# Performance work log

Measured on AMD Instinct MI355X. Metric: run time of the kernel, lower is better.

Reference implementation:

```python
import jax, jax.numpy as jnp
import numpy as np

B, D, H, L, A, NH = 32768, 512, 512, 64, 4, 4
HD = L // NH  # head dim
TEMPS = jnp.array([1.5, 0.5, 1.0, 0.8], dtype=jnp.float32)  # explorer/exploiter/validator/integrator


def setup_inputs() -> dict:
    key = jax.random.key(0)
    ks = jax.random.split(key, 32)
    s = 0.05
    n = lambda k, shp: jax.random.normal(k, shp, dtype=jnp.float32) * s
    return {
        'x': jax.random.normal(ks[0], (B, D), dtype=jnp.float32),
        'eps': jax.random.normal(ks[1], (B, A, L), dtype=jnp.float32),
        'W1': n(ks[2], (H, D)), 'b1': n(ks[3], (H,)),
        'W2': n(ks[4], (H, H)), 'b2': n(ks[5], (H,)),
        'muW': n(ks[6], (A, L, H)), 'mub': n(ks[7], (A, L)),
        'lvW': n(ks[8], (A, L, H)), 'lvb': n(ks[9], (A, L)),
        'Wqkv': n(ks[10], (3 * L, L)), 'bqkv': n(ks[11], (3 * L,)),
        'Wo': n(ks[12], (L, L)), 'bo': n(ks[13], (L,)),
        'Wc': n(ks[14], (L, A * L)), 'bc': n(ks[15], (L,)),
        'Wd1': n(ks[16], (H, L)), 'bd1': n(ks[17], (H,)),
        'Wd2': n(ks[18], (H, H)), 'bd2': n(ks[19], (H,)),
        'Wd3': n(ks[20], (D, H)), 'bd3': n(ks[21], (D,)),
    }


def reference(x, eps, W1, b1, W2, b2, muW, mub, lvW, lvb,
              Wqkv, bqkv, Wo, bo, Wc, bc, Wd1, bd1, Wd2, bd2, Wd3, bd3):
    b = x.shape[0]
    # shared encoder backbone: Linear-ReLU-Linear-ReLU
    h = jax.nn.relu(x @ W1.T + b1)
    h = jax.nn.relu(h @ W2.T + b2)
    # per-agent heads, batched over agent axis a
    mus = jnp.einsum('bh,alh->bal', h, muW) + mub                      # (B,A,L)
    logvars = jnp.einsum('bh,alh->bal', h, lvW) + lvb + jnp.log(TEMPS)[:, None]
    std = jnp.exp(0.5 * logvars)
    z = mus + eps * std * TEMPS[:, None]                               # (B,A,L)
    # multihead self-attention across the A agents (seq_len = A)
    qkv = z @ Wqkv.T + bqkv                                            # (B,A,3L)
    q, k, v = jnp.split(qkv, 3, axis=-1)
    q = q.reshape(b, A, NH, HD)
    k = k.reshape(b, A, NH, HD)
    v = v.reshape(b, A, NH, HD)
    scores = jnp.einsum('bqnh,bknh->bnqk', q, k) / jnp.sqrt(jnp.float32(HD))
    attn = jax.nn.softmax(scores, axis=-1)
    ctx = jnp.einsum('bnqk,bknh->bqnh', attn, v).reshape(b, A, L)
    z_att = ctx @ Wo.T + bo                                            # (B,A,L)
    # consensus over flattened agent latents
    z_consensus = z_att.reshape(b, A * L) @ Wc.T + bc                  # (B,L)

    def decode(zz):
        d = jax.nn.relu(zz @ Wd1.T + bd1)
        d = jax.nn.relu(d @ Wd2.T + bd2)
        return d @ Wd3.T + bd3

    x_recon = decode(z_consensus)                                      # (B,D)
    agent_recons = decode(z)                                           # (B,A,D)
    # stack consensus recon with per-agent recons: (B, A+1, D)
    return jnp.concatenate([x_recon[:, None, :], agent_recons], axis=1)
```

## Files before the change

kernel.cpp:

```cpp
#include <hip/hip_runtime.h>

typedef __bf16 bf16_t;
typedef __bf16 bf16x8 __attribute__((ext_vector_type(8)));
typedef __bf16 bf16x4 __attribute__((ext_vector_type(4)));
typedef float  f32x4  __attribute__((ext_vector_type(4)));
typedef float  f32x16 __attribute__((ext_vector_type(16)));

#define MFMA16(a,b,c) __builtin_amdgcn_mfma_f32_16x16x32_bf16((a),(b),(c),0,0,0)
#define MFMA32(a,b,c) __builtin_amdgcn_mfma_f32_32x32x16_bf16((a),(b),(c),0,0,0)
#define GLOBAL_AS __attribute__((address_space(1)))
#define LDS_AS    __attribute__((address_space(3)))
#define MEMFENCE  asm volatile("" ::: "memory")

__device__ __forceinline__ int act_off(int row, int kByte) {
    int byte = (row << 10) + kByte;
    return byte ^ ((row & 15) << 4);
}

__device__ __forceinline__ bf16x8 lds_read8(const bf16_t* base, int row, int k, int rowB) {
    int byte = row * rowB + (k << 1);
    byte ^= ((row & 7) << 4);
    return *(const bf16x8*)((const char*)base + byte);
}
__device__ __forceinline__ void lds_write8B(bf16_t* base, int row, int col, int rowB, bf16x4 v) {
    int byte = row * rowB + (col << 1);
    byte ^= ((row & 7) << 4);
    *(bf16x4*)((char*)base + byte) = v;
}
__device__ __forceinline__ bf16x4 lds_read8B(const bf16_t* base, int row, int col, int rowB) {
    int byte = row * rowB + (col << 1);
    byte ^= ((row & 7) << 4);
    return *(const bf16x4*)((const char*)base + byte);
}
__device__ __forceinline__ void lds_write1(bf16_t* base, int row, int col, int rowB, float v) {
    int byte = row * rowB + (col << 1);
    byte ^= ((row & 7) << 4);
    *(bf16_t*)((char*)base + byte) = (bf16_t)v;
}
__device__ __forceinline__ void lds_write16B(bf16_t* base, int row, int colbyte, int rowB, bf16x8 v) {
    int byte = row * rowB + colbyte;
    byte ^= ((row & 7) << 4);
    *(bf16x8*)((char*)base + byte) = v;
}
__device__ __forceinline__ bf16x8 lds_read16B(const bf16_t* base, int row, int colbyte, int rowB) {
    int byte = row * rowB + colbyte;
    byte ^= ((row & 7) << 4);
    return *(const bf16x8*)((const char*)base + byte);
}

__device__ __forceinline__ void gload_lds16(const void* g, void* l) {
    __builtin_amdgcn_global_load_lds((const GLOBAL_AS void*)g, (LDS_AS void*)l, 16, 0, 0);
}

__device__ __forceinline__ void stageW32(const bf16_t* __restrict__ Wt, int tile,
                                         char* wbuf, int bufIdx, int wave, int lane) {
    const char* s = (const char*)Wt + (size_t)tile * 32768 + wave * 4096 + lane * 16;
    char* d = wbuf + bufIdx * 32768 + wave * 4096;
#pragma unroll
    for (int c = 0; c < 4; ++c)
        gload_lds16(s + c * 1024, d + c * 1024);
}

template<int NS, bool CONT, int TB>
__device__ __forceinline__ void layer_gl(f32x4 (&acc)[4][4],
    const bf16_t* act, char* wbuf,
    const bf16_t* __restrict__ Wt, const bf16_t* __restrict__ Wn,
    int wave, int lane, int n0, int l15, int lhi)
{
#pragma unroll
    for (int s = 0; s < NS; ++s) {
        if (s == NS - 1 && !CONT) {
            asm volatile("s_waitcnt vmcnt(0)" ::: "memory");
        } else {
            asm volatile("s_waitcnt vmcnt(4)" ::: "memory");
        }
        __builtin_amdgcn_s_barrier();
        if (s + 2 < NS)  stageW32(Wt, s + 2,      wbuf, (TB + s + 2) % 3, wave, lane);
        else if (CONT)   stageW32(Wn, s + 2 - NS, wbuf, (TB + s + 2) % 3, wave, lane);
        const char* bb = wbuf + ((TB + s) % 3) * 32768 + lhi * 8192;
        bf16x8 a[4], b[4];
#pragma unroll
        for (int cf = 0; cf < 4; ++cf)
            b[cf] = *(const bf16x8*)(bb + (n0 + cf * 16 + l15) * 16);
#pragma unroll
        for (int rf = 0; rf < 4; ++rf)
            a[rf] = lds_read8(act, rf * 16 + l15, s * 32 + lhi * 8, 1024);
#pragma unroll
        for (int rf = 0; rf < 4; ++rf)
#pragma unroll
            for (int cf = 0; cf < 4; ++cf)
                acc[rf][cf] = MFMA16(b[cf], a[rf], acc[rf][cf]);
    }
}

__device__ __forceinline__ void zero4(f32x4 (&acc)[4][4]) {
#pragma unroll
    for (int rf = 0; rf < 4; ++rf)
#pragma unroll
        for (int cf = 0; cf < 4; ++cf)
            acc[rf][cf] = f32x4{0.f, 0.f, 0.f, 0.f};
}

template<bool RELU>
__device__ __forceinline__ void epi_lds16(const f32x4 (&acc)[4][4], const float* __restrict__ bias,
    bf16_t* dst, int n0, int l15, int lhi)
{
#pragma unroll
    for (int cf = 0; cf < 4; ++cf) {
        const int c0 = n0 + cf * 16 + lhi * 4;
        float4 b4 = *(const float4*)(bias + c0);
#pragma unroll
        for (int rf = 0; rf < 4; ++rf) {
            float v0 = acc[rf][cf][0] + b4.x;
            float v1 = acc[rf][cf][1] + b4.y;
            float v2 = acc[rf][cf][2] + b4.z;
            float v3 = acc[rf][cf][3] + b4.w;
            if (RELU) {
                v0 = fmaxf(v0, 0.f); v1 = fmaxf(v1, 0.f);
                v2 = fmaxf(v2, 0.f); v3 = fmaxf(v3, 0.f);
            }
            bf16x4 p = { (bf16_t)v0, (bf16_t)v1, (bf16_t)v2, (bf16_t)v3 };
            lds_write8B(dst, rf * 16 + l15, c0, 1024, p);
        }
    }
}

__device__ __forceinline__ void compute_step(f32x16 (&acc)[2][4],
    const bf16_t* act, const char* wbuf, int s, int wm, int wn, int l31, int kg)
{
    bf16x8 a[2], b[4];
#pragma unroll
    for (int cc = 0; cc < 4; ++cc)
        b[cc] = *(const bf16x8*)(wbuf + kg * 8192 + (wn * 128 + cc * 32 + l31) * 16);
#pragma unroll
    for (int rr = 0; rr < 2; ++rr)
        a[rr] = *(const bf16x8*)((const char*)act +
                    act_off(wm * 64 + rr * 32 + l31, s * 32 + kg * 16));
#pragma unroll
    for (int rr = 0; rr < 2; ++rr)
#pragma unroll
        for (int cc = 0; cc < 4; ++cc)
            acc[rr][cc] = MFMA32(b[cc], a[rr], acc[rr][cc]);
}

template<int NS>
__device__ __forceinline__ void layer_rs(f32x16 (&acc)[2][4],
    const bf16_t* act, char* wbuf, const bf16_t* __restrict__ Wt,
    int t, int wave, int lane, int wm, int wn, int l31, int kg)
{
    const char* gb = (const char*)Wt;
    {
        const char* s0 = gb + wave * 2048 + lane * 16;
        char* d0 = wbuf + wave * 2048;
        gload_lds16(s0, d0);
        gload_lds16(s0 + 1024, d0 + 1024);
    }
    MEMFENCE;
    uint4 rA0, rA1, rB0, rB1;
    rA0 = *(const uint4*)(gb + 16384 + t * 16);
    rA1 = *(const uint4*)(gb + 16384 + 8192 + t * 16);
    asm volatile("s_waitcnt vmcnt(0)" ::: "memory");
    __builtin_amdgcn_s_barrier();

#pragma unroll
    for (int p = 0; p < NS / 2; ++p) {
        {
            const int s = 2 * p;
            compute_step(acc, act, wbuf + (s & 1) * 16384, s, wm, wn, l31, kg);
            if (s + 2 < NS) {
                MEMFENCE;
                rB0 = *(const uint4*)(gb + (size_t)(s + 2) * 16384 + t * 16);
                rB1 = *(const uint4*)(gb + (size_t)(s + 2) * 16384 + 8192 + t * 16);
                MEMFENCE;
            }
            if (s + 1 < NS) {
                if (s + 2 < NS) asm volatile("s_waitcnt vmcnt(2)" ::: "memory");
                else            asm volatile("s_waitcnt vmcnt(0)" ::: "memory");
                char* nb = wbuf + ((s + 1) & 1) * 16384;
                *(uint4*)(nb + t * 16) = rA0;
                *(uint4*)(nb + 8192 + t * 16) = rA1;
                asm volatile("s_waitcnt lgkmcnt(0)" ::: "memory");
            }
            __builtin_amdgcn_s_barrier();
        }
        {
            const int s = 2 * p + 1;
            compute_step(acc, act, wbuf + (s & 1) * 16384, s, wm, wn, l31, kg);
            if (s + 2 < NS) {
                MEMFENCE;
                rA0 = *(const uint4*)(gb + (size_t)(s + 2) * 16384 + t * 16);
                rA1 = *(const uint4*)(gb + (size_t)(s + 2) * 16384 + 8192 + t * 16);
                MEMFENCE;
            }
            if (s + 1 < NS) {
                if (s + 2 < NS) asm volatile("s_waitcnt vmcnt(2)" ::: "memory");
                else            asm volatile("s_waitcnt vmcnt(0)" ::: "memory");
                char* nb = wbuf + ((s + 1) & 1) * 16384;
                *(uint4*)(nb + t * 16) = rB0;
                *(uint4*)(nb + 8192 + t * 16) = rB1;
                asm volatile("s_waitcnt lgkmcnt(0)" ::: "memory");
            }
            __builtin_amdgcn_s_barrier();
        }
    }
}

__device__ __forceinline__ void zero32(f32x16 (&acc)[2][4]) {
#pragma unroll
    for (int rr = 0; rr < 2; ++rr)
#pragma unroll
        for (int cc = 0; cc < 4; ++cc)
#pragma unroll
            for (int i = 0; i < 16; ++i) acc[rr][cc][i] = 0.f;
}

template<bool RELU>
__device__ __forceinline__ void epi_lds32(const f32x16 (&acc)[2][4], const float* __restrict__ bias,
    bf16_t* act, int wm, int wn, int l31, int kg)
{
#pragma unroll
    for (int cc = 0; cc < 4; ++cc)
#pragma unroll
    for (int q = 0; q < 4; ++q) {
        const int c0 = wn * 128 + cc * 32 + q * 8 + kg * 4;
        float4 b4 = *(const float4*)(bias + c0);
#pragma unroll
        for (int rr = 0; rr < 2; ++rr) {
            float v0 = acc[rr][cc][q * 4 + 0] + b4.x;
            float v1 = acc[rr][cc][q * 4 + 1] + b4.y;
            float v2 = acc[rr][cc][q * 4 + 2] + b4.z;
            float v3 = acc[rr][cc][q * 4 + 3] + b4.w;
            if (RELU) {
                v0 = fmaxf(v0, 0.f); v1 = fmaxf(v1, 0.f);
                v2 = fmaxf(v2, 0.f); v3 = fmaxf(v3, 0.f);
            }
            bf16x4 p = { (bf16_t)v0, (bf16_t)v1, (bf16_t)v2, (bf16_t)v3 };
            *(bf16x4*)((char*)act + act_off(wm * 64 + rr * 32 + l31, c0 * 2)) = p;
        }
    }
}
__device__ __forceinline__ void epi_global32(const f32x16 (&acc)[2][4], const float* __restrict__ bias,
    float* __restrict__ out, long r0, int wm, int wn, int l31, int kg)
{
#pragma unroll
    for (int cc = 0; cc < 4; ++cc)
#pragma unroll
    for (int q = 0; q < 4; ++q) {
        const int c0 = wn * 128 + cc * 32 + q * 8 + kg * 4;
        float4 b4 = *(const float4*)(bias + c0);
#pragma unroll
        for (int rr = 0; rr < 2; ++rr) {
            float4 o = { acc[rr][cc][q * 4 + 0] + b4.x, acc[rr][cc][q * 4 + 1] + b4.y,
                         acc[rr][cc][q * 4 + 2] + b4.z, acc[rr][cc][q * 4 + 3] + b4.w };
            *(float4*)(out + (r0 + wm * 64 + rr * 32 + l31) * 512 + c0) = o;
        }
    }
}

__device__ __forceinline__ void decode32(int m, int& n, int& k) {
    int s = m >> 14, r = m & 16383;
    int kg = r >> 12, q = r & 4095;
    n = q >> 3;
    k = (s << 5) + (kg << 3) + (q & 7);
}
__device__ __forceinline__ void decode16(int m, int& n, int& k) {
    int s = m >> 13, r = m & 8191;
    int kg = r >> 12, q = r & 4095;
    n = q >> 3;
    k = (s << 4) + (kg << 3) + (q & 7);
}
__global__ __launch_bounds__(256) void cast_kernel(
    const float* __restrict__ W1, const float* __restrict__ W2,
    const float* __restrict__ muW, const float* __restrict__ lvW,
    const float* __restrict__ Wqkv, const float* __restrict__ Wo,
    const float* __restrict__ Wc, const float* __restrict__ Wd1,
    const float* __restrict__ Wd2, const float* __restrict__ Wd3,
    bf16_t* __restrict__ dst)
{
    int i = blockIdx.x * 256 + threadIdx.x;
    float val;
    int n, k;
    if (i < 262144) {
        decode32(i, n, k);                    val = W1[n * 512 + k];
    } else if (i < 524288) {
        decode32(i - 262144, n, k);           val = W2[n * 512 + k];
    } else if (i < 786432) {
        decode32(i - 524288, n, k);
        val = (n < 256) ? muW[n * 512 + k] : lvW[(n - 256) * 512 + k];
    } else if (i < 798720) { val = Wqkv[i - 786432]; }
    else if (i < 802816)   { val = Wo[i - 798720]; }
    else if (i < 819200)   { val = Wc[i - 802816]; }
    else if (i < 851968) {
        decode16(i - 819200, n, k);           val = Wd1[n * 64 + k];
    } else if (i < 1114112) {
        decode16(i - 851968, n, k);           val = Wd2[n * 512 + k];
    } else {
        decode16(i - 1114112, n, k);          val = Wd3[n * 512 + k];
    }
    dst[i] = (bf16_t)val;
}

__global__ __launch_bounds__(512, 2) void enc_kernel(
    const float* __restrict__ x, const float* __restrict__ eps,
    const bf16_t* __restrict__ W1t, const float* __restrict__ b1,
    const bf16_t* __restrict__ W2t, const float* __restrict__ b2,
    const bf16_t* __restrict__ Ht,  const float* __restrict__ mub,
    const float* __restrict__ lvb,  bf16_t* __restrict__ zout)
{
    __shared__ bf16_t act[64 * 512];
    __shared__ alignas(16) char wbuf[3 * 32768];
    const int t = threadIdx.x;
    const int wave = t >> 6, lane = t & 63, l15 = lane & 15, lhi = lane >> 4;
    const int n0 = wave * 64;
    const size_t r0 = (size_t)blockIdx.x * 64;

    stageW32(W1t, 0, wbuf, 0, wave, lane);
    stageW32(W1t, 1, wbuf, 1, wave, lane);

    for (int it = 0; it < 16; ++it) {
        int flat = it * 512 + t;
        int row = flat >> 7, c4 = flat & 127;
        float4 v = ((const float4*)(x + (r0 + row) * 512))[c4];
        bf16x4 h = { (bf16_t)v.x, (bf16_t)v.y, (bf16_t)v.z, (bf16_t)v.w };
        int byte = (row << 10) + (c4 << 3);
        byte ^= ((row & 7) << 4);
        *(bf16x4*)((char*)act + byte) = h;
    }
    asm volatile("s_waitcnt lgkmcnt(0)" ::: "memory");

    f32x4 acc[4][4];
    zero4(acc);
    layer_gl<16, true, 0>(acc, act, wbuf, W1t, W2t, wave, lane, n0, l15, lhi);
    __builtin_amdgcn_s_barrier();
    epi_lds16<true>(acc, b1, act, n0, l15, lhi);
    asm volatile("s_waitcnt lgkmcnt(0)" ::: "memory");
    __builtin_amdgcn_s_barrier();

    zero4(acc);
    layer_gl<16, true, 1>(acc, act, wbuf, W2t, Ht, wave, lane, n0, l15, lhi);
    __builtin_amdgcn_s_barrier();
    epi_lds16<true>(acc, b2, act, n0, l15, lhi);
    asm volatile("s_waitcnt lgkmcnt(0)" ::: "memory");
    __builtin_amdgcn_s_barrier();

    zero4(acc);
    layer_gl<16, false, 2>(acc, act, wbuf, Ht, (const bf16_t*)nullptr, wave, lane, n0, l15, lhi);
    __builtin_amdgcn_s_barrier();
    epi_lds16<false>(acc, (n0 < 256) ? (mub + 0) : (lvb - 256), act, n0, l15, lhi);
    asm volatile("s_waitcnt lgkmcnt(0)" ::: "memory");
    __builtin_amdgcn_s_barrier();

    const int cc = (t & 63) * 4;
    const int ag = cc >> 6;
    const float tp = (ag == 0) ? 1.8371173070873836f
                   : (ag == 1) ? 0.35355339059327373f
                   : (ag == 2) ? 1.0f
                               : 0.7155417527999327f;
    const int rb = t >> 6;
    for (int it = 0; it < 8; ++it) {
        int row = it * 8 + rb;
        bf16x4 mu4 = lds_read8B(act, row, cc, 1024);
        bf16x4 lv4 = lds_read8B(act, row, cc + 256, 1024);
        float4 ep4 = *(const float4*)(eps + (r0 + row) * 256 + cc);
        bf16x4 zo;
        zo[0] = (bf16_t)fmaf(ep4.x * tp, expf(0.5f * (float)lv4[0]), (float)mu4[0]);
        zo[1] = (bf16_t)fmaf(ep4.y * tp, expf(0.5f * (float)lv4[1]), (float)mu4[1]);
        zo[2] = (bf16_t)fmaf(ep4.z * tp, expf(0.5f * (float)lv4[2]), (float)mu4[2]);
        zo[3] = (bf16_t)fmaf(ep4.w * tp, expf(0.5f * (float)lv4[3]), (float)mu4[3]);
        *(bf16x4*)(zout + (r0 + row) * 256 + cc) = zo;
    }
}

__global__ __launch_bounds__(512) void attn_kernel(
    const bf16_t* __restrict__ z,
    const bf16_t* __restrict__ Wqkvb, const float* __restrict__ bqkv,
    const bf16_t* __restrict__ Wob,   const float* __restrict__ bo,
    const bf16_t* __restrict__ Wcb,   const float* __restrict__ bc,
    bf16_t* __restrict__ zcb)
{
    __shared__ bf16_t zt[256 * 64];
    __shared__ bf16_t qt[256 * 192];
    const int t = threadIdx.x;
    const size_t s0 = (size_t)blockIdx.x * 64;

    for (int it = 0; it < 4; ++it) {
        int ch = it * 512 + t;
        int r = ch >> 3, cc = ch & 7;
        bf16x8 v = *(const bf16x8*)(z + s0 * 256 + r * 64 + cc * 8);
        lds_write16B(zt, r, cc * 16, 128, v);
    }
    __syncthreads();
    const int wave = t >> 6, lane = t & 63, l15 = lane & 15, lhi = lane >> 4;
    const int rbase = wave * 32;

    for (int cc = 0; cc < 4; ++cc) {
        f32x4 acc[2][3] = {};
#pragma unroll
        for (int ks = 0; ks < 2; ++ks) {
            int k = ks * 32 + lhi * 8;
            bf16x8 a0 = lds_read8(zt, rbase + l15, k, 128);
            bf16x8 a1 = lds_read8(zt, rbase + 16 + l15, k, 128);
#pragma unroll
            for (int cf = 0; cf < 3; ++cf) {
                bf16x8 b = *(const bf16x8*)(Wqkvb + (cc * 48 + cf * 16 + l15) * 64 + k);
                acc[0][cf] = MFMA16(a0, b, acc[0][cf]);
                acc[1][cf] = MFMA16(a1, b, acc[1][cf]);
            }
        }
#pragma unroll
        for (int cf = 0; cf < 3; ++cf) {
            int col = cc * 48 + cf * 16 + l15;
            float bs = bqkv[col];
#pragma unroll
            for (int rf = 0; rf < 2; ++rf)
#pragma unroll
                for (int r = 0; r < 4; ++r)
                    lds_write1(qt, rbase + rf * 16 + lhi * 4 + r, col, 384, acc[rf][cf][r] + bs);
        }
    }
    __syncthreads();

    if (t < 256) {
        const int sl = t >> 2, head = t & 3;
        bf16x8 qv[4][2], kv[4][2], vv[4][2];
#pragma unroll
        for (int a2 = 0; a2 < 4; ++a2) {
            int r = sl * 4 + a2;
#pragma unroll
            for (int i = 0; i < 2; ++i) {
                qv[a2][i] = lds_read16B(qt, r, head * 32 + 16 * i, 384);
                kv[a2][i] = lds_read16B(qt, r, 128 + head * 32 + 16 * i, 384);
                vv[a2][i] = lds_read16B(qt, r, 256 + head * 32 + 16 * i, 384);
            }
        }
        float sc[4][4];
#pragma unroll
        for (int qa = 0; qa < 4; ++qa)
#pragma unroll
            for (int ka = 0; ka < 4; ++ka) {
                float s = 0.f;
#pragma unroll
                for (int i = 0; i < 2; ++i)
#pragma unroll
                    for (int j = 0; j < 8; ++j)
                        s += (float)qv[qa][i][j] * (float)kv[ka][i][j];
                sc[qa][ka] = s * 0.25f;
            }
#pragma unroll
        for (int qa = 0; qa < 4; ++qa) {
            float m = fmaxf(fmaxf(sc[qa][0], sc[qa][1]), fmaxf(sc[qa][2], sc[qa][3]));
            float e[4], sum = 0.f;
#pragma unroll
            for (int ka = 0; ka < 4; ++ka) { e[ka] = expf(sc[qa][ka] - m); sum += e[ka]; }
            float inv = 1.f / sum;
#pragma unroll
            for (int i = 0; i < 2; ++i) {
                bf16x8 cv;
#pragma unroll
                for (int j = 0; j < 8; ++j) {
                    float cval = 0.f;
#pragma unroll
                    for (int ka = 0; ka < 4; ++ka) cval += e[ka] * inv * (float)vv[ka][i][j];
                    cv[j] = (bf16_t)cval;
                }
                lds_write16B(zt, sl * 4 + qa, head * 32 + 16 * i, 128, cv);
            }
        }
    }
    __syncthreads();

    {
        f32x4 acc[2][4] = {};
#pragma unroll
        for (int ks = 0; ks < 2; ++ks) {
            int k = ks * 32 + lhi * 8;
            bf16x8 a0 = lds_read8(zt, rbase + l15, k, 128);
            bf16x8 a1 = lds_read8(zt, rbase + 16 + l15, k, 128);
#pragma unroll
            for (int cf = 0; cf < 4; ++cf) {
                bf16x8 b = *(const bf16x8*)(Wob + (cf * 16 + l15) * 64 + k);
                acc[0][cf] = MFMA16(a0, b, acc[0][cf]);
                acc[1][cf] = MFMA16(a1, b, acc[1][cf]);
            }
        }
        __syncthreads();
#pragma unroll
        for (int cf = 0; cf < 4; ++cf) {
            int col = cf * 16 + l15;
            float bs = bo[col];
#pragma unroll
            for (int rf = 0; rf < 2; ++rf)
#pragma unroll
                for (int r = 0; r < 4; ++r)
                    lds_write1(qt, rbase + rf * 16 + lhi * 4 + r, col, 128, acc[rf][cf][r] + bs);
        }
    }
    __syncthreads();

    {
        f32x4 acc2[2] = {};
        const int rfw = wave >> 1, cbase = (wave & 1) * 2;
        const int srow = rfw * 16 + l15;
#pragma unroll
        for (int ks = 0; ks < 8; ++ks) {
            int k = ks * 32 + lhi * 8;
            int byte = (srow << 9) + (k << 1);
            byte ^= ((((srow << 2) + (k >> 6)) & 7) << 4);
            bf16x8 a = *(const bf16x8*)((const char*)qt + byte);
#pragma unroll
            for (int i = 0; i < 2; ++i) {
                bf16x8 b = *(const bf16x8*)(Wcb + ((cbase + i) * 16 + l15) * 256 + k);
                acc2[i] = MFMA16(a, b, acc2[i]);
            }
        }
#pragma unroll
        for (int i = 0; i < 2; ++i) {
            int col = (cbase + i) * 16 + l15;
            float bs = bc[col];
#pragma unroll
            for (int r = 0; r < 4; ++r) {
                int s = (int)(s0) + rfw * 16 + lhi * 4 + r;
                zcb[(size_t)s * 64 + col] = (bf16_t)(acc2[i][r] + bs);
            }
        }
    }
}

__global__ __launch_bounds__(512, 2) void dec_kernel(
    const bf16_t* __restrict__ z, const bf16_t* __restrict__ zc,
    const bf16_t* __restrict__ Wd1t, const float* __restrict__ bd1,
    const bf16_t* __restrict__ Wd2t, const float* __restrict__ bd2,
    const bf16_t* __restrict__ Wd3t, const float* __restrict__ bd3,
    float* __restrict__ out)
{
    __shared__ bf16_t act[128 * 512];
    __shared__ alignas(16) char wbuf[2 * 16384];
    const int t = threadIdx.x;
    const int wave = t >> 6, lane = t & 63, l31 = lane & 31, kg = lane >> 5;
    const int wm = wave >> 2, wn = wave & 3;
    const long r0 = (long)blockIdx.x * 128;

    for (int it = 0; it < 2; ++it) {
        int flat = it * 512 + t;
        int row = flat >> 3, ch = flat & 7;
        long rg = r0 + row;
        int s5 = (int)(rg / 5), j = (int)(rg - (long)s5 * 5);
        const bf16_t* src = (j == 0) ? (zc + (size_t)s5 * 64)
                                     : (z + (size_t)s5 * 256 + (j - 1) * 64);
        bf16x8 v = *(const bf16x8*)(src + ch * 8);
        *(bf16x8*)((char*)act + act_off(row, ch * 16)) = v;
    }
    asm volatile("s_waitcnt lgkmcnt(0)" ::: "memory");

    f32x16 acc[2][4];
    zero32(acc);
    layer_rs<4>(acc, act, wbuf, Wd1t, t, wave, lane, wm, wn, l31, kg);
    epi_lds32<true>(acc, bd1, act, wm, wn, l31, kg);
    asm volatile("s_waitcnt lgkmcnt(0)" ::: "memory");
    __builtin_amdgcn_s_barrier();

    zero32(acc);
    layer_rs<32>(acc, act, wbuf, Wd2t, t, wave, lane, wm, wn, l31, kg);
    epi_lds32<true>(acc, bd2, act, wm, wn, l31, kg);
    asm volatile("s_waitcnt lgkmcnt(0)" ::: "memory");
    __builtin_amdgcn_s_barrier();

    zero32(acc);
    layer_rs<32>(acc, act, wbuf, Wd3t, t, wave, lane, wm, wn, l31, kg);
    epi_global32(acc, bd3, out, r0, wm, wn, l31, kg);
}

extern "C" void kernel_launch(void* const* d_in, const int* in_sizes, int n_in,
                              void* d_out, int out_size, void* d_ws, size_t ws_size,
                              hipStream_t stream) {
    const float* x    = (const float*)d_in[0];
    const float* eps  = (const float*)d_in[1];
    const float* W1   = (const float*)d_in[2];
    const float* b1   = (const float*)d_in[3];
    const float* W2   = (const float*)d_in[4];
    const float* b2   = (const float*)d_in[5];
    const float* muW  = (const float*)d_in[6];
    const float* mub  = (const float*)d_in[7];
    const float* lvW  = (const float*)d_in[8];
    const float* lvb  = (const float*)d_in[9];
    const float* Wqkv = (const float*)d_in[10];
    const float* bqkv = (const float*)d_in[11];
    const float* Wo   = (const float*)d_in[12];
    const float* bo   = (const float*)d_in[13];
    const float* Wc   = (const float*)d_in[14];
    const float* bc   = (const float*)d_in[15];
    const float* Wd1  = (const float*)d_in[16];
    const float* bd1  = (const float*)d_in[17];
    const float* Wd2  = (const float*)d_in[18];
    const float* bd2  = (const float*)d_in[19];
    const float* Wd3  = (const float*)d_in[20];
    const float* bd3  = (const float*)d_in[21];
    float* out = (float*)d_out;

    bf16_t* wsb  = (bf16_t*)d_ws;
    bf16_t* W1t  = wsb + 0;
    bf16_t* W2t  = wsb + 262144;
    bf16_t* Ht   = wsb + 524288;
    bf16_t* Wqkvb= wsb + 786432;
    bf16_t* Wob  = wsb + 798720;
    bf16_t* Wcb  = wsb + 802816;
    bf16_t* Wd1t = wsb + 819200;
    bf16_t* Wd2t = wsb + 851968;
    bf16_t* Wd3t = wsb + 1114112;
    bf16_t* zbuf = wsb + 1376256;
    bf16_t* zcb  = wsb + 9764864;

    cast_kernel<<<dim3(5376), dim3(256), 0, stream>>>(
        W1, W2, muW, lvW, Wqkv, Wo, Wc, Wd1, Wd2, Wd3, wsb);
    enc_kernel<<<dim3(512), dim3(512), 0, stream>>>(
        x, eps, W1t, b1, W2t, b2, Ht, mub, lvb, zbuf);
    attn_kernel<<<dim3(512), dim3(512), 0, stream>>>(
        zbuf, Wqkvb, bqkv, Wob, bo, Wcb, bc, zcb);
    dec_kernel<<<dim3(1280), dim3(512), 0, stream>>>(
        zbuf, zcb, Wd1t, bd1, Wd2t, bd2, Wd3t, bd3, out);
}
```

Baseline: 380.8 us.

## Stream decoder weights directly into registers instead of staging through LDS

The decoder kernel no longer stages each weight K-slice through a double-buffered LDS buffer with per-step barriers. Each wave now loads its own B fragments from global memory straight into registers, two slices ahead, in a layout the cast kernel pre-permutes to match. This removes the LDS weight traffic, the per-step block barriers and 32KB of LDS. In exchange each wave issues its own global loads (duplicated across the two wm waves) and holds more registers, which may hurt latency hiding or occupancy.

```diff
diff --git a/kernel.cpp b/kernel.cpp
--- a/kernel.cpp
+++ b/kernel.cpp
@@ -10,7 +10,6 @@
 #define MFMA32(a,b,c) __builtin_amdgcn_mfma_f32_32x32x16_bf16((a),(b),(c),0,0,0)
 #define GLOBAL_AS __attribute__((address_space(1)))
 #define LDS_AS    __attribute__((address_space(3)))
-#define MEMFENCE  asm volatile("" ::: "memory")
 
 __device__ __forceinline__ int act_off(int row, int kByte) {
     int byte = (row << 10) + kByte;
@@ -125,13 +124,10 @@
     }
 }
 
-__device__ __forceinline__ void compute_step(f32x16 (&acc)[2][4],
-    const bf16_t* act, const char* wbuf, int s, int wm, int wn, int l31, int kg)
-{
-    bf16x8 a[2], b[4];
-#pragma unroll
-    for (int cc = 0; cc < 4; ++cc)
-        b[cc] = *(const bf16x8*)(wbuf + kg * 8192 + (wn * 128 + cc * 32 + l31) * 16);
+__device__ __forceinline__ void dec_mfma(f32x16 (&acc)[2][4],
+    const bf16_t* act, const bf16x8 (&b)[4], int s, int wm, int l31, int kg)
+{
+    bf16x8 a[2];
 #pragma unroll
     for (int rr = 0; rr < 2; ++rr)
         a[rr] = *(const bf16x8*)((const char*)act +
@@ -144,63 +140,41 @@
 }
 
 template<int NS>
-__device__ __forceinline__ void layer_rs(f32x16 (&acc)[2][4],
-    const bf16_t* act, char* wbuf, const bf16_t* __restrict__ Wt,
-    int t, int wave, int lane, int wm, int wn, int l31, int kg)
-{
-    const char* gb = (const char*)Wt;
-    {
-        const char* s0 = gb + wave * 2048 + lane * 16;
-        char* d0 = wbuf + wave * 2048;
-        gload_lds16(s0, d0);
-        gload_lds16(s0 + 1024, d0 + 1024);
-    }
-    MEMFENCE;
-    uint4 rA0, rA1, rB0, rB1;
-    rA0 = *(const uint4*)(gb + 16384 + t * 16);
-    rA1 = *(const uint4*)(gb + 16384 + 8192 + t * 16);
-    asm volatile("s_waitcnt vmcnt(0)" ::: "memory");
-    __builtin_amdgcn_s_barrier();
-
+__device__ __forceinline__ void layer_reg(f32x16 (&acc)[2][4],
+    const bf16_t* act, const bf16_t* __restrict__ Wt,
+    int lane, int wm, int wn, int l31, int kg)
+{
+    const char* gb = (const char*)Wt + wn * 4096 + lane * 16;
+    bf16x8 pA[4], pB[4];
+#pragma unroll
+    for (int c = 0; c < 4; ++c) pA[c] = *(const bf16x8*)(gb + c * 1024);
+#pragma unroll
+    for (int c = 0; c < 4; ++c) pB[c] = *(const bf16x8*)(gb + 16384 + c * 1024);
 #pragma unroll
     for (int p = 0; p < NS / 2; ++p) {
         {
             const int s = 2 * p;
-            compute_step(acc, act, wbuf + (s & 1) * 16384, s, wm, wn, l31, kg);
+            bf16x8 b[4];
+#pragma unroll
+            for (int c = 0; c < 4; ++c) b[c] = pA[c];
             if (s + 2 < NS) {
-                MEMFENCE;
-                rB0 = *(const uint4*)(gb + (size_t)(s + 2) * 16384 + t * 16);
-                rB1 = *(const uint4*)(gb + (size_t)(s + 2) * 16384 + 8192 + t * 16);
-                MEMFENCE;
-            }
-            if (s + 1 < NS) {
-                if (s + 2 < NS) asm volatile("s_waitcnt vmcnt(2)" ::: "memory");
-                else            asm volatile("s_waitcnt vmcnt(0)" ::: "memory");
-                char* nb = wbuf + ((s + 1) & 1) * 16384;
-                *(uint4*)(nb + t * 16) = rA0;
-                *(uint4*)(nb + 8192 + t * 16) = rA1;
-                asm volatile("s_waitcnt lgkmcnt(0)" ::: "memory");
-            }
-            __builtin_amdgcn_s_barrier();
+#pragma unroll
+                for (int c = 0; c < 4; ++c)
+                    pA[c] = *(const bf16x8*)(gb + (size_t)(s + 2) * 16384 + c * 1024);
+            }
+            dec_mfma(acc, act, b, s, wm, l31, kg);
         }
         {
             const int s = 2 * p + 1;
-            compute_step(acc, act, wbuf + (s & 1) * 16384, s, wm, wn, l31, kg);
+            bf16x8 b[4];
+#pragma unroll
+            for (int c = 0; c < 4; ++c) b[c] = pB[c];
             if (s + 2 < NS) {
-                MEMFENCE;
-                rA0 = *(const uint4*)(gb + (size_t)(s + 2) * 16384 + t * 16);
-                rA1 = *(const uint4*)(gb + (size_t)(s + 2) * 16384 + 8192 + t * 16);
-                MEMFENCE;
-            }
-            if (s + 1 < NS) {
-                if (s + 2 < NS) asm volatile("s_waitcnt vmcnt(2)" ::: "memory");
-                else            asm volatile("s_waitcnt vmcnt(0)" ::: "memory");
-                char* nb = wbuf + ((s + 1) & 1) * 16384;
-                *(uint4*)(nb + t * 16) = rB0;
-                *(uint4*)(nb + 8192 + t * 16) = rB1;
-                asm volatile("s_waitcnt lgkmcnt(0)" ::: "memory");
-            }
-            __builtin_amdgcn_s_barrier();
+#pragma unroll
+                for (int c = 0; c < 4; ++c)
+                    pB[c] = *(const bf16x8*)(gb + (size_t)(s + 2) * 16384 + c * 1024);
+            }
+            dec_mfma(acc, act, b, s, wm, l31, kg);
         }
     }
 }
@@ -263,11 +237,11 @@
     n = q >> 3;
     k = (s << 5) + (kg << 3) + (q & 7);
 }
-__device__ __forceinline__ void decode16(int m, int& n, int& k) {
-    int s = m >> 13, r = m & 8191;
-    int kg = r >> 12, q = r & 4095;
-    n = q >> 3;
-    k = (s << 4) + (kg << 3) + (q & 7);
+__device__ __forceinline__ void decode_reg(int m, int& n, int& k) {
+    int tile = m >> 13, e = m & 8191;
+    int wn = e >> 11, c = (e >> 9) & 3, ln = (e >> 3) & 63, j = e & 7;
+    n = wn * 128 + c * 32 + (ln & 31);
+    k = (tile << 4) + ((ln >> 5) << 3) + j;
 }
 __global__ __launch_bounds__(256) void cast_kernel(
     const float* __restrict__ W1, const float* __restrict__ W2,
@@ -291,11 +265,11 @@
     else if (i < 802816)   { val = Wo[i - 798720]; }
     else if (i < 819200)   { val = Wc[i - 802816]; }
     else if (i < 851968) {
-        decode16(i - 819200, n, k);           val = Wd1[n * 64 + k];
+        decode_reg(i - 819200, n, k);         val = Wd1[n * 64 + k];
     } else if (i < 1114112) {
-        decode16(i - 851968, n, k);           val = Wd2[n * 512 + k];
+        decode_reg(i - 851968, n, k);         val = Wd2[n * 512 + k];
     } else {
-        decode16(i - 1114112, n, k);          val = Wd3[n * 512 + k];
+        decode_reg(i - 1114112, n, k);        val = Wd3[n * 512 + k];
     }
     dst[i] = (bf16_t)val;
 }
@@ -534,7 +508,6 @@
     float* __restrict__ out)
 {
     __shared__ bf16_t act[128 * 512];
-    __shared__ alignas(16) char wbuf[2 * 16384];
     const int t = threadIdx.x;
     const int wave = t >> 6, lane = t & 63, l31 = lane & 31, kg = lane >> 5;
     const int wm = wave >> 2, wn = wave & 3;
@@ -550,23 +523,25 @@
         bf16x8 v = *(const bf16x8*)(src + ch * 8);
         *(bf16x8*)((char*)act + act_off(row, ch * 16)) = v;
     }
-    asm volatile("s_waitcnt lgkmcnt(0)" ::: "memory");
+    __syncthreads();
 
     f32x16 acc[2][4];
     zero32(acc);
-    layer_rs<4>(acc, act, wbuf, Wd1t, t, wave, lane, wm, wn, l31, kg);
+    layer_reg<4>(acc, act, Wd1t, lane, wm, wn, l31, kg);
+    __builtin_amdgcn_s_barrier();
     epi_lds32<true>(acc, bd1, act, wm, wn, l31, kg);
     asm volatile("s_waitcnt lgkmcnt(0)" ::: "memory");
     __builtin_amdgcn_s_barrier();
 
     zero32(acc);
-    layer_rs<32>(acc, act, wbuf, Wd2t, t, wave, lane, wm, wn, l31, kg);
+    layer_reg<32>(acc, act, Wd2t, lane, wm, wn, l31, kg);
+    __builtin_amdgcn_s_barrier();
     epi_lds32<true>(acc, bd2, act, wm, wn, l31, kg);
     asm volatile("s_waitcnt lgkmcnt(0)" ::: "memory");
     __builtin_amdgcn_s_barrier();
 
     zero32(acc);
-    layer_rs<32>(acc, act, wbuf, Wd3t, t, wave, lane, wm, wn, l31, kg);
+    layer_reg<32>(acc, act, Wd3t, lane, wm, wn, l31, kg);
     epi_global32(acc, bd3, out, r0, wm, wn, l31, kg);
 }
 
```

Result: faster. 352.0 us (-7.6%).
